# Kernel optimization log

Hardware: AMD Instinct MI355X
Metric: run time of the kernel (lower is better)

The kernel has to match this reference:

```python
import jax, jax.numpy as jnp
import numpy as np

L = 20        # num layers (TTS LM)
Q = 512       # query length
PAST = 512    # past_kv_len
END = PAST + Q  # end_step = 1024
MAXS = 2048   # max_seq_len
D = 896       # hidden size
NKV = 2       # KV heads
NQ = 14       # Q heads
G = NQ // NKV # GQA repeat = 7
HD = 64       # head dim
FF = 4864     # SwiGLU intermediate (Qwen2.5-0.5B)
EPS = 1e-6
SCALE = 1.0 / np.sqrt(HD)


def rms_norm(x, w):
    return x * jax.lax.rsqrt(jnp.mean(x * x, axis=-1, keepdims=True) + EPS) * w


def rotate_half(x):
    x1, x2 = jnp.split(x, 2, axis=-1)
    return jnp.concatenate([-x2, x1], axis=-1)


def setup_inputs() -> dict:
    key = jax.random.key(0)
    ks = jax.random.split(key, 24)
    s = 0.02
    inp = {
        'hidden_states': jax.random.normal(ks[0], (1, Q, D), jnp.float32),
        'position_cos': jax.random.uniform(ks[1], (1, Q, HD), jnp.float32, -1.0, 1.0),
        'position_sin': jax.random.uniform(ks[2], (1, Q, HD), jnp.float32, -1.0, 1.0),
        'attention_mask': jnp.zeros((1, 1, Q, END), jnp.float32),
        'inject_mode': jnp.zeros((1,), jnp.float32),
        'inject_k': jax.random.normal(ks[3], (1, L * NKV, Q, HD), jnp.float32),
        'inject_v': jax.random.normal(ks[4], (1, L * NKV, Q, HD), jnp.float32),
        'k_cache': (jax.random.normal(ks[5], (L, 1, NKV, MAXS, HD), jnp.float32) * 0.5).astype(jnp.float16),
        'v_cache': (jax.random.normal(ks[6], (L, 1, NKV, MAXS, HD), jnp.float32) * 0.5).astype(jnp.float16),
        'Wq': jax.random.normal(ks[7], (L, D, NQ * HD), jnp.float32) * s,
        'bq': jax.random.normal(ks[8], (L, NQ * HD), jnp.float32) * s,
        'Wk': jax.random.normal(ks[9], (L, D, NKV * HD), jnp.float32) * s,
        'bk': jax.random.normal(ks[10], (L, NKV * HD), jnp.float32) * s,
        'Wv': jax.random.normal(ks[11], (L, D, NKV * HD), jnp.float32) * s,
        'bv': jax.random.normal(ks[12], (L, NKV * HD), jnp.float32) * s,
        'Wo': jax.random.normal(ks[13], (L, NQ * HD, D), jnp.float32) * s,
        'ln1': jnp.ones((L, D), jnp.float32),
        'ln2': jnp.ones((L, D), jnp.float32),
        'Wg': jax.random.normal(ks[14], (L, D, FF), jnp.float32) * s,
        'Wu': jax.random.normal(ks[15], (L, D, FF), jnp.float32) * s,
        'Wd': jax.random.normal(ks[16], (L, FF, D), jnp.float32) * s,
        'final_w': jnp.ones((D,), jnp.float32),
    }
    return inp


def reference(hidden_states, position_cos, position_sin, attention_mask,
              inject_mode, inject_k, inject_v, k_cache, v_cache,
              Wq, bq, Wk, bk, Wv, bv, Wo, ln1, ln2, Wg, Wu, Wd, final_w):
    cos = position_cos[:, None]   # [1,1,Q,HD]
    sin = position_sin[:, None]
    inj = inject_mode[0]
    normal = 1.0 - inj
    mask = attention_mask[:, None]  # [1,1,1,Q,END] broadcast over (g,h)
    # per-layer inject slices: [L,1,NKV,Q,HD]
    ik = jnp.transpose(inject_k.reshape(1, L, NKV, Q, HD), (1, 0, 2, 3, 4))
    iv = jnp.transpose(inject_v.reshape(1, L, NKV, Q, HD), (1, 0, 2, 3, 4))

    def layer_fn(h, p):
        (wq, bq_, wk, bk_, wv, bv_, wo, l1, l2, wg, wu, wd, kc, vc, ikl, ivl) = p
        residual = h
        x = rms_norm(h, l1)
        q = (x @ wq + bq_).reshape(1, Q, NQ, HD).transpose(0, 2, 1, 3)   # [1,NQ,Q,HD]
        k = (x @ wk + bk_).reshape(1, Q, NKV, HD).transpose(0, 2, 1, 3)  # [1,NKV,Q,HD]
        v = (x @ wv + bv_).reshape(1, Q, NKV, HD).transpose(0, 2, 1, 3)
        q = q * cos + rotate_half(q) * sin
        k = k * cos + rotate_half(k) * sin
        k = normal * k + inj * ikl
        v = normal * v + inj * ivl
        kc = kc.at[:, :, PAST:END].set(k.astype(jnp.float16))
        vc = vc.at[:, :, PAST:END].set(v.astype(jnp.float16))
        kf = kc[:, :, :END].astype(jnp.float32)  # [1,NKV,END,HD]
        vf = vc[:, :, :END].astype(jnp.float32)
        qg = q.reshape(1, NKV, G, Q, HD)         # grouped GQA (== repeat_kv)
        scores = jnp.einsum('bghqd,bgkd->bghqk', qg, kf) * SCALE + mask
        w = jax.nn.softmax(scores, axis=-1)
        o = jnp.einsum('bghqk,bgkd->bghqd', w, vf)
        o = o.reshape(1, NQ, Q, HD).transpose(0, 2, 1, 3).reshape(1, Q, NQ * HD)
        h = residual + o @ wo
        residual = h
        x = rms_norm(h, l2)
        h = residual + (jax.nn.silu(x @ wg) * (x @ wu)) @ wd
        return h, None

    xs = (Wq, bq, Wk, bk, Wv, bv, Wo, ln1, ln2, Wg, Wu, Wd, k_cache, v_cache, ik, iv)
    h, _ = jax.lax.scan(layer_fn, hidden_states, xs)
    return rms_norm(h, final_w)
```

## Files before the change

kernel.cpp:

```cpp
#include <hip/hip_runtime.h>
#include <hip/hip_fp16.h>
#include <hip/hip_cooperative_groups.h>

namespace cg = cooperative_groups;

#define NLAYER 20
#define QLEN 512
#define PAST 512
#define ENDS 1024
#define MAXS 2048
#define DMODEL 896
#define NKV 2
#define NQ 14
#define GQ 7
#define HD 64
#define FF 4864
#define RMSEPS 1e-6f
#define ATT_SCALE 0.125f

typedef _Float16 f16x8 __attribute__((ext_vector_type(8)));
typedef float f32x4 __attribute__((ext_vector_type(4)));
typedef unsigned int u32_;

__device__ __forceinline__ void gld16(const void* g, void* l) {
    __builtin_amdgcn_global_load_lds(
        (const __attribute__((address_space(1))) u32_*)g,
        (__attribute__((address_space(3))) u32_*)l, 16, 0, 0);
}

union SmemU {
    struct { __half As[8192]; __half Bs[8192]; } g;
    struct { __half S[16512]; float rowinv[16]; } a;
    struct { float T[32][33]; } p;
    struct { float red[4]; } r;
};

__device__ __forceinline__ void gemm_body(
    const __half* __restrict__ A, int lda, const __half* __restrict__ B, int ldb,
    float* __restrict__ outP, __half* __restrict__ actP, int N, int Kps, int mode,
    int bx, int by, int bz, int t, __half* As, __half* Bs)
{
    const int lane = t & 63, wave = t >> 6;
    const int wm = wave >> 1, wn = wave & 1;
    const int m0 = by * 128, n0 = bx * 128;
    const int kb0 = bz * Kps;
    const int sr = t >> 2, sc = (t & 3) * 8;
    const int la = lane & 15, ka = (lane >> 4) * 8;
    const int nIter = Kps >> 5;
    const int swzS = ((sr >> 1) & 3) << 3;
    const int scw = sc ^ swzS;
    const size_t a0 = (size_t)(m0 + sr) * lda + kb0 + scw;
    const size_t a1 = (size_t)(m0 + sr + 64) * lda + kb0 + scw;
    const size_t b0 = (size_t)(n0 + sr) * ldb + kb0 + scw;
    const size_t b1 = (size_t)(n0 + sr + 64) * ldb + kb0 + scw;
    const int l0 = sr * 32 + sc, l1 = (sr + 64) * 32 + sc;

    f32x4 acc[4][4] = {};
    gld16(&A[a0], &As[l0]);
    gld16(&A[a1], &As[l1]);
    gld16(&B[b0], &Bs[l0]);
    gld16(&B[b1], &Bs[l1]);
    int buf = 0;
    for (int kt = 0; kt < nIter; kt++) {
        __syncthreads();
        if (kt + 1 < nIter) {
            const int ko = (kt + 1) * 32;
            gld16(&A[a0 + ko], &As[(buf ^ 1) * 4096 + l0]);
            gld16(&A[a1 + ko], &As[(buf ^ 1) * 4096 + l1]);
            gld16(&B[b0 + ko], &Bs[(buf ^ 1) * 4096 + l0]);
            gld16(&B[b1 + ko], &Bs[(buf ^ 1) * 4096 + l1]);
        }
        f16x8 av[4], bv[4];
#pragma unroll
        for (int i = 0; i < 4; i++) {
            const int row = wm * 64 + i * 16 + la;
            av[i] = *(const f16x8*)&As[buf * 4096 + row * 32 + (ka ^ (((row >> 1) & 3) << 3))];
        }
#pragma unroll
        for (int j = 0; j < 4; j++) {
            const int row = wn * 64 + j * 16 + la;
            bv[j] = *(const f16x8*)&Bs[buf * 4096 + row * 32 + (ka ^ (((row >> 1) & 3) << 3))];
        }
#pragma unroll
        for (int i = 0; i < 4; i++)
#pragma unroll
            for (int j = 0; j < 4; j++)
                acc[i][j] = __builtin_amdgcn_mfma_f32_16x16x32_f16(av[i], bv[j], acc[i][j], 0, 0, 0);
        buf ^= 1;
    }
    __syncthreads();
    const int r0 = m0 + wm * 64 + (lane >> 4) * 4;
    const int c0 = n0 + wn * 64 + la;
    if (mode == 0) {
        float* o = outP + (size_t)bz * QLEN * N;
#pragma unroll
        for (int i = 0; i < 4; i++)
#pragma unroll
            for (int j = 0; j < 4; j++)
#pragma unroll
                for (int r = 0; r < 4; r++)
                    o[(size_t)(r0 + i * 16 + r) * N + c0 + j * 16] = acc[i][j][r];
    } else {
#pragma unroll
        for (int i = 0; i < 4; i++)
#pragma unroll
            for (int j = 0; j < 4; j++)
#pragma unroll
                for (int r = 0; r < 4; r++) {
                    float v = acc[i][j][r];
                    float other = __shfl_xor(v, 1);
                    if (!(la & 1)) {
                        const int c = c0 + j * 16;
                        const int row = r0 + i * 16 + r;
                        float sg = v / (1.f + __expf(-v));
                        actP[(size_t)row * FF + (c >> 1)] = __float2half(sg * other);
                    }
                }
    }
}

__device__ __forceinline__ void prep_body(
    const float* __restrict__ Wq, const float* __restrict__ Wk, const float* __restrict__ Wv,
    const float* __restrict__ Wo, const float* __restrict__ Wg, const float* __restrict__ Wu,
    const float* __restrict__ Wd, int layer, int z, int bx, int t, float (*T)[33],
    __half* __restrict__ dstW)
{
    const int K = (z == 3) ? FF : DMODEL;
    const int N = (z == 0) ? 1152 : (z == 2) ? 2 * FF : DMODEL;
    const int tilesN = N / 32;
    const int tk = bx / tilesN, tn = bx % tilesN;
    const int k0 = tk * 32, n0 = tn * 32;
    const float* src; int ldn, nc0; int isU = 0;
    if (z == 0) {
        if (n0 < 896)       { src = Wq + (size_t)layer * 896 * 896; ldn = 896; nc0 = n0; }
        else if (n0 < 1024) { src = Wk + (size_t)layer * 896 * 128; ldn = 128; nc0 = n0 - 896; }
        else                { src = Wv + (size_t)layer * 896 * 128; ldn = 128; nc0 = n0 - 1024; }
    } else if (z == 1) { src = Wo + (size_t)layer * 896 * 896; ldn = 896; nc0 = n0; }
    else if (z == 2) {
        if (n0 < FF) { src = Wg + (size_t)layer * 896 * FF; ldn = FF; nc0 = n0; }
        else         { src = Wu + (size_t)layer * 896 * FF; ldn = FF; nc0 = n0 - FF; isU = 1; }
    } else { src = Wd + (size_t)layer * FF * 896; ldn = 896; nc0 = n0; }

    __syncthreads();
    const int r = t >> 3, c4 = (t & 7) * 4;
    float4 v = *(const float4*)&src[(size_t)(k0 + r) * ldn + nc0 + c4];
    T[r][c4 + 0] = v.x; T[r][c4 + 1] = v.y; T[r][c4 + 2] = v.z; T[r][c4 + 3] = v.w;
    __syncthreads();
    const int drow = (z == 2) ? (2 * (nc0 + r) + isU) : (n0 + r);
    __half* dst = dstW + (size_t)drow * K + k0 + c4;
    __half2 p0 = __halves2half2(__float2half_rn(T[c4 + 0][r]), __float2half_rn(T[c4 + 1][r]));
    __half2 p1 = __halves2half2(__float2half_rn(T[c4 + 2][r]), __float2half_rn(T[c4 + 3][r]));
    *(__half2*)dst = p0;
    *(__half2*)(dst + 2) = p1;
    __syncthreads();
}

__device__ __forceinline__ void prep_dispatch(
    const float* Wq, const float* Wk, const float* Wv, const float* Wo,
    const float* Wg, const float* Wu, const float* Wd,
    const float* bq, const float* bk, const float* bv,
    int layer, int j, int t, float (*T)[33],
    __half* wq, __half* wo, __half* wgu, __half* wd, float* bqkv)
{
    int z; __half* dst; int bx = j;
    if (j < 1008)       { z = 0; dst = wq; }
    else if (j < 1792)  { z = 1; dst = wo;  bx -= 1008; }
    else if (j < 10304) { z = 2; dst = wgu; bx -= 1792; }
    else                { z = 3; dst = wd;  bx -= 10304; }
    prep_body(Wq, Wk, Wv, Wo, Wg, Wu, Wd, layer, z, bx, t, T, dst);
    if (z == 0 && bx == 0) {
        for (int i = t; i < 1152; i += 256) {
            float b = (i < 896) ? bq[(size_t)layer * 896 + i]
                    : (i < 1024) ? bk[(size_t)layer * 128 + i - 896]
                                 : bv[(size_t)layer * 128 + i - 1024];
            bqkv[i] = b;
        }
    }
}

__device__ __forceinline__ void ropekv_body(
    const float* __restrict__ part, const float* __restrict__ bias,
    const float* __restrict__ cosb, const float* __restrict__ sinb,
    const float* __restrict__ injm, const float* __restrict__ injk,
    const float* __restrict__ injv, const float* __restrict__ kc32,
    const float* __restrict__ vc32, int layer, int nsplit,
    __half* __restrict__ qr, __half* __restrict__ Ka, __half* __restrict__ Vt,
    int p, int lt)
{
    const int kvh = lt >> 6, d = lt & 63;
    if (p < PAST) {
        const size_t idx = (((size_t)layer * NKV + kvh) * MAXS + p) * HD + d;
        Ka[((size_t)kvh * ENDS + p) * HD + d] = __float2half(kc32[idx]);
        Vt[((size_t)kvh * HD + d) * ENDS + p] = __float2half(vc32[idx]);
        return;
    }
    const int pn = p - PAST;
    const float inj = injm[0], nrm = 1.f - inj;
    const float* rb = part + (size_t)pn * 1152;
    const size_t sst = (size_t)QLEN * 1152;
    auto rsum = [&](int c) {
        float x = bias[c];
        for (int s = 0; s < nsplit; s++) x += rb[(size_t)s * sst + c];
        return x;
    };
    for (int idx = lt; idx < NQ * HD; idx += 128) {
        const int dd = idx & 63;
        float x = rsum(idx);
        int pc = (dd < 32) ? idx + 32 : idx - 32;
        float pv = rsum(pc);
        if (dd < 32) pv = -pv;
        float rv = x * cosb[pn * HD + dd] + pv * sinb[pn * HD + dd];
        qr[((size_t)(idx >> 6) * QLEN + pn) * HD + dd] = __float2half(rv);
    }
    {
        const int c = NQ * HD + lt;
        float x = rsum(c);
        int pc = (d < 32) ? c + 32 : c - 32;
        float pv = rsum(pc);
        if (d < 32) pv = -pv;
        float rv = x * cosb[pn * HD + d] + pv * sinb[pn * HD + d];
        float kn = nrm * rv + inj * injk[(((size_t)layer * NKV + kvh) * QLEN + pn) * HD + d];
        Ka[((size_t)kvh * ENDS + PAST + pn) * HD + d] = __float2half(kn);
        const int cv = NQ * HD + NKV * HD + lt;
        float vv = rsum(cv);
        float vn = nrm * vv + inj * injv[(((size_t)layer * NKV + kvh) * QLEN + pn) * HD + d];
        Vt[((size_t)kvh * HD + d) * ENDS + PAST + pn] = __float2half(vn);
    }
}

__device__ __forceinline__ int sswz(int row, int col) {
    return row * 1032 + (col ^ ((row & 7) << 3));
}

__device__ __forceinline__ void attn_body(
    const __half* __restrict__ qr, const __half* __restrict__ Ka,
    const __half* __restrict__ Vt, const float* __restrict__ mask,
    __half* __restrict__ ob, int q0, int h, int t, __half* S, float* rowinv)
{
    const int kv = h / GQ;
    const int lane = t & 63, w = t >> 6;
    const int la = lane & 15, kg = lane >> 4;

    const f16x8* qp = (const f16x8*)&qr[((size_t)h * QLEN + q0 + la) * HD + kg * 8];
    const f16x8 qa0 = qp[0], qa1 = qp[4];
    __syncthreads();

    for (int kb = 0; kb < 256; kb += 16) {
        const int key = w * 256 + kb + la;
        const f16x8* kp = (const f16x8*)&Ka[((size_t)kv * ENDS + key) * HD + kg * 8];
        f32x4 s4 = {0.f, 0.f, 0.f, 0.f};
        s4 = __builtin_amdgcn_mfma_f32_16x16x32_f16(qa0, kp[0], s4, 0, 0, 0);
        s4 = __builtin_amdgcn_mfma_f32_16x16x32_f16(qa1, kp[4], s4, 0, 0, 0);
#pragma unroll
        for (int r = 0; r < 4; r++) {
            const int row = kg * 4 + r;
            float sv = s4[r] * ATT_SCALE + mask[(size_t)(q0 + row) * ENDS + key];
            S[sswz(row, key)] = __float2half(sv);
        }
    }
    __syncthreads();
    {
        const int row = w * 4 + kg;
        float mx = -1e30f;
        for (int j = 0; j < 64; j++)
            mx = fmaxf(mx, __half2float(S[sswz(row, la + 16 * j)]));
        for (int o = 1; o < 16; o <<= 1) mx = fmaxf(mx, __shfl_xor(mx, o));
        float sum = 0.f;
        for (int j = 0; j < 64; j++) {
            const int idx = sswz(row, la + 16 * j);
            float e = __expf(__half2float(S[idx]) - mx);
            S[idx] = __float2half(e);
            sum += e;
        }
        for (int o = 1; o < 16; o <<= 1) sum += __shfl_xor(sum, o);
        if (la == 0) rowinv[row] = 1.f / sum;
    }
    __syncthreads();
    {
        const int d = 16 * w + la;
        const __half* vrow = &Vt[((size_t)kv * HD + d) * ENDS];
        f32x4 acc = {0.f, 0.f, 0.f, 0.f};
        for (int ks = 0; ks < ENDS; ks += 32) {
            f16x8 pa = *(const f16x8*)&S[sswz(la, ks + kg * 8)];
            f16x8 vb = *(const f16x8*)&vrow[ks + kg * 8];
            acc = __builtin_amdgcn_mfma_f32_16x16x32_f16(pa, vb, acc, 0, 0, 0);
        }
#pragma unroll
        for (int r = 0; r < 4; r++) {
            const int qrow = kg * 4 + r;
            ob[(size_t)(q0 + qrow) * (NQ * HD) + h * HD + d] =
                __float2half(acc[r] * rowinv[qrow]);
        }
    }
    __syncthreads();
}

__device__ inline void cvt_store(float* p, float v)  { *p = v; }
__device__ inline void cvt_store(__half* p, float v) { *p = __float2half(v); }

template <typename OUT>
__device__ __forceinline__ void rms_body(
    float* __restrict__ h, const float* __restrict__ parts, int nparts,
    const float* __restrict__ w, OUT* __restrict__ out, int m, int t,
    float* red, float scale)
{
    float loc[4];
    float ss = 0.f;
    int r = 0;
    for (int i = t; i < DMODEL; i += 256, r++) {
        float x = h[(size_t)m * DMODEL + i];
        for (int s = 0; s < nparts; s++)
            x += parts[(size_t)s * QLEN * DMODEL + (size_t)m * DMODEL + i];
        loc[r] = x;
        if (nparts) h[(size_t)m * DMODEL + i] = x;
        ss += x * x;
    }
    for (int o = 32; o; o >>= 1) ss += __shfl_xor(ss, o);
    if ((t & 63) == 0) red[t >> 6] = ss;
    __syncthreads();
    float rs = rsqrtf((red[0] + red[1] + red[2] + red[3]) / (float)DMODEL + RMSEPS);
    r = 0;
    for (int i = t; i < DMODEL; i += 256, r++)
        cvt_store(&out[(size_t)m * DMODEL + i], loc[r] * rs * w[i] * scale);
    __syncthreads();
}

struct P22 {
    const float *hidden, *cosb, *sinb, *mask, *injm, *injk, *injv, *kc32, *vc32;
    const float *Wq, *bq, *Wk, *bk, *Wv, *bv, *Wo, *ln1, *ln2, *Wg, *Wu, *Wd, *finw;
    float *h; __half *xn, *qr, *Ka, *Vt, *ob, *act; float *BIGR;
    float *bqkv0, *bqkv1;
    __half *wq0, *wo0, *wgu0, *wd0, *wq1, *wo1, *wgu1, *wd1;
    float *outF;
};

#define PC_RMS1 512
#define PC_QKV  880
#define PC_ROPE 512
#define PC_ATTN 2304
#define PC_O    1824
#define PC_RMS2 1024
#define PC_GU   5904
#define PC_D    1600
#define PB_RMS1 0
#define PB_QKV  512
#define PB_ROPE 1392
#define PB_ATTN 1904
#define PB_O    4208
#define PB_RMS2 6032
#define PB_GU   7056
#define PB_D    12960

__global__ __launch_bounds__(256) void mega_kernel(P22 P)
{
    __shared__ SmemU sm;
    cg::grid_group gg = cg::this_grid();
    const int nb = gridDim.x, bid = blockIdx.x, t = threadIdx.x;

    for (int j = bid; j < 1792; j += nb) {
        int i = j * 256 + t;
        if (i < QLEN * DMODEL) P.h[i] = P.hidden[i];
    }
    for (int j = bid; j < 14560; j += nb)
        prep_dispatch(P.Wq, P.Wk, P.Wv, P.Wo, P.Wg, P.Wu, P.Wd, P.bq, P.bk, P.bv,
                      0, j, t, sm.p.T, P.wq0, P.wo0, P.wgu0, P.wd0, P.bqkv0);
    gg.sync();

    for (int l = 0; l < NLAYER; l++) {
        const int pb = l & 1;
        const __half* wq  = pb ? P.wq1  : P.wq0;
        const __half* wo  = pb ? P.wo1  : P.wo0;
        const __half* wgu = pb ? P.wgu1 : P.wgu0;
        const __half* wd  = pb ? P.wd1  : P.wd0;
        const float*  bqk = pb ? P.bqkv1 : P.bqkv0;
        const bool hasN = (l + 1 < NLAYER);
        __half* nwq  = pb ? P.wq0  : P.wq1;
        __half* nwo  = pb ? P.wo0  : P.wo1;
        __half* nwgu = pb ? P.wgu0 : P.wgu1;
        __half* nwd  = pb ? P.wd0  : P.wd1;
        float*  nbq  = pb ? P.bqkv0 : P.bqkv1;
        #define PREPN(idx) prep_dispatch(P.Wq, P.Wk, P.Wv, P.Wo, P.Wg, P.Wu, P.Wd, \
            P.bq, P.bk, P.bv, l + 1, (idx), t, sm.p.T, nwq, nwo, nwgu, nwd, nbq)

        for (int j = bid; j < QLEN + (hasN ? PC_RMS1 : 0); j += nb) {
            if (j < QLEN)
                rms_body<__half>(P.h, l ? P.BIGR : nullptr, l ? 8 : 0,
                                 P.ln1 + (size_t)l * DMODEL, P.xn, j, t, sm.r.red, 1.f);
            else PREPN(PB_RMS1 + j - QLEN);
        }
        gg.sync();

        for (int j = bid; j < 144 + (hasN ? PC_QKV : 0); j += nb) {
            if (j < 144) {
                int z = j / 36, r = j % 36;
                gemm_body(P.xn, DMODEL, wq, DMODEL, P.BIGR, nullptr, 1152, 224, 0,
                          r % 9, r / 9, z, t, sm.g.As, sm.g.Bs);
            } else PREPN(PB_QKV + j - 144);
        }
        gg.sync();

        for (int j = bid; j < 512 + (hasN ? PC_ROPE : 0); j += nb) {
            if (j < 512)
                ropekv_body(P.BIGR, bqk, P.cosb, P.sinb, P.injm, P.injk, P.injv,
                            P.kc32, P.vc32, l, 4, P.qr, P.Ka, P.Vt,
                            j * 2 + (t >> 7), t & 127);
            else PREPN(PB_ROPE + j - 512);
        }
        gg.sync();

        for (int j = bid; j < 448 + (hasN ? PC_ATTN : 0); j += nb) {
            if (j < 448)
                attn_body(P.qr, P.Ka, P.Vt, P.mask, P.ob, (j & 31) * 16, j >> 5, t,
                          sm.a.S, sm.a.rowinv);
            else PREPN(PB_ATTN + j - 448);
        }
        gg.sync();

        for (int j = bid; j < 112 + (hasN ? PC_O : 0); j += nb) {
            if (j < 112) {
                int z = j / 28, r = j % 28;
                gemm_body(P.ob, DMODEL, wo, DMODEL, P.BIGR, nullptr, DMODEL, 224, 0,
                          r % 7, r / 7, z, t, sm.g.As, sm.g.Bs);
            } else PREPN(PB_O + j - 112);
        }
        gg.sync();

        for (int j = bid; j < QLEN + (hasN ? PC_RMS2 : 0); j += nb) {
            if (j < QLEN)
                rms_body<__half>(P.h, P.BIGR, 4, P.ln2 + (size_t)l * DMODEL, P.xn,
                                 j, t, sm.r.red, 1.f);
            else PREPN(PB_RMS2 + j - QLEN);
        }
        gg.sync();

        for (int j = bid; j < 304 + (hasN ? PC_GU : 0); j += nb) {
            if (j < 304)
                gemm_body(P.xn, DMODEL, wgu, DMODEL, nullptr, P.act, 2 * FF, DMODEL, 1,
                          j % 76, j / 76, 0, t, sm.g.As, sm.g.Bs);
            else PREPN(PB_GU + j - 304);
        }
        gg.sync();

        for (int j = bid; j < 224 + (hasN ? PC_D : 0); j += nb) {
            if (j < 224) {
                int z = j / 28, r = j % 28;
                gemm_body(P.act, FF, wd, FF, P.BIGR, nullptr, DMODEL, 608, 0,
                          r % 7, r / 7, z, t, sm.g.As, sm.g.Bs);
            } else PREPN(PB_D + j - 224);
        }
        gg.sync();
        #undef PREPN
    }
    for (int j = bid; j < QLEN; j += nb)
        rms_body<float>(P.h, P.BIGR, 8, P.finw, P.outF, j, t, sm.r.red, 1.f);
}

__global__ __launch_bounds__(256) void init_kernel(
    const float* __restrict__ hidden, float* __restrict__ h, int* __restrict__ flags)
{
    const int idx = blockIdx.x * 256 + threadIdx.x;
    if (blockIdx.x == 0 && threadIdx.x < 8) flags[threadIdx.x] = 0;
    if (idx < QLEN * DMODEL) h[idx] = hidden[idx];
}

__global__ __launch_bounds__(256) void prep_all(
    const float* Wq, const float* Wk, const float* Wv, const float* Wo,
    const float* Wg, const float* Wu, const float* Wd,
    const float* bq, const float* bk, const float* bv, int layer,
    __half* wqkv, __half* wo, __half* wgu, __half* wd, float* bqkv)
{
    __shared__ float T[32][33];
    prep_dispatch(Wq, Wk, Wv, Wo, Wg, Wu, Wd, bq, bk, bv, layer, blockIdx.x,
                  threadIdx.x, T, wqkv, wo, wgu, wd, bqkv);
}

__global__ __launch_bounds__(256) void gemm128(
    const __half* A, int lda, const __half* B, int ldb,
    float* outP, __half* actP, int N, int Kps, int mode)
{
    __shared__ SmemU sm;
    gemm_body(A, lda, B, ldb, outP, actP, N, Kps, mode,
              blockIdx.x, blockIdx.y, blockIdx.z, threadIdx.x, sm.g.As, sm.g.Bs);
}

__global__ __launch_bounds__(128) void ropekv_kernel(
    const float* part, const float* bias, const float* cosb, const float* sinb,
    const float* injm, const float* injk, const float* injv,
    const float* kc32, const float* vc32, int layer, int nsplit,
    __half* qr, __half* Ka, __half* Vt)
{
    ropekv_body(part, bias, cosb, sinb, injm, injk, injv, kc32, vc32,
                layer, nsplit, qr, Ka, Vt, blockIdx.x, threadIdx.x);
}

__global__ __launch_bounds__(256) void attn_mfma(
    const __half* qr, const __half* Ka, const __half* Vt, const float* mask, __half* ob)
{
    __shared__ SmemU sm;
    attn_body(qr, Ka, Vt, mask, ob, blockIdx.x * 16, blockIdx.y, threadIdx.x,
              sm.a.S, sm.a.rowinv);
}

template <typename OUT>
__global__ __launch_bounds__(256) void rms_kernel(
    float* h, const float* parts, int nparts, const float* w, OUT* out,
    const int* flags)
{
    __shared__ float red[4];
    float scale = 1.f;
    if (flags) {
        int E = flags[1];
        for (int i = 0; i < E; i++) scale *= 3.f;
    }
    rms_body<OUT>(h, parts, nparts, w, out, blockIdx.x, threadIdx.x, red, scale);
}

__global__ __launch_bounds__(256) void check_gemm(
    const __half* A, int lda, const __half* B, int K,
    const float* part, int N, int nz, int* flags)
{
    const int t = threadIdx.x;
    const int m = (t >> 4) * 33;
    const int n = ((t & 15) * 997) % N;
    float acc = 0.f;
    for (int k = 0; k < K; k++)
        acc += __half2float(A[(size_t)m * lda + k]) * __half2float(B[(size_t)n * K + k]);
    float got = 0.f;
    for (int z = 0; z < nz; z++) got += part[(size_t)z * QLEN * N + (size_t)m * N + n];
    if (fabsf(acc - got) > 0.03f) atomicOr(&flags[1], 1);
}

extern "C" void kernel_launch(void* const* d_in, const int* in_sizes, int n_in,
                              void* d_out, int out_size, void* d_ws, size_t ws_size,
                              hipStream_t stream)
{
    const float*  hidden = (const float*)d_in[0];
    const float*  cosb   = (const float*)d_in[1];
    const float*  sinb   = (const float*)d_in[2];
    const float*  mask   = (const float*)d_in[3];
    const float*  injm   = (const float*)d_in[4];
    const float*  injk   = (const float*)d_in[5];
    const float*  injv   = (const float*)d_in[6];
    const float*  kc32   = (const float*)d_in[7];
    const float*  vc32   = (const float*)d_in[8];
    const float*  Wq     = (const float*)d_in[9];
    const float*  bq     = (const float*)d_in[10];
    const float*  Wk     = (const float*)d_in[11];
    const float*  bk     = (const float*)d_in[12];
    const float*  Wv     = (const float*)d_in[13];
    const float*  bv     = (const float*)d_in[14];
    const float*  Wo     = (const float*)d_in[15];
    const float*  ln1    = (const float*)d_in[16];
    const float*  ln2    = (const float*)d_in[17];
    const float*  Wg     = (const float*)d_in[18];
    const float*  Wu     = (const float*)d_in[19];
    const float*  Wd     = (const float*)d_in[20];
    const float*  finw   = (const float*)d_in[21];

    bool size_ok = (n_in == 22) &&
        in_sizes[0] == 458752 && in_sizes[1] == 32768 && in_sizes[3] == 524288 &&
        in_sizes[4] == 1 && in_sizes[5] == 1310720 && in_sizes[7] == 5242880 &&
        in_sizes[9] == 16056320 && in_sizes[10] == 17920 && in_sizes[11] == 2293760 &&
        in_sizes[15] == 16056320 && in_sizes[16] == 17920 && in_sizes[18] == 87162880 &&
        in_sizes[20] == 87162880 && in_sizes[21] == 896;
    if (!size_ok) { hipMemsetAsync(d_out, 0x42, (size_t)out_size * 4, stream); return; }

    char* ws = (char*)d_ws;
    size_t off = 0;
    auto alloc = [&](size_t bytes) { void* p = ws + off; off += (bytes + 255) & ~255ull; return p; };
    int*    flags = (int*)alloc(256);
    float*  bqkv0 = (float*)alloc(1152 * 4);
    float*  bqkv1 = (float*)alloc(1152 * 4);
    float*  h     = (float*)alloc((size_t)QLEN * DMODEL * 4);
    __half* xn    = (__half*)alloc((size_t)QLEN * DMODEL * 2);
    __half* qr    = (__half*)alloc((size_t)NQ * QLEN * HD * 2);
    __half* Ka    = (__half*)alloc((size_t)NKV * ENDS * HD * 2);
    __half* Vt    = (__half*)alloc((size_t)NKV * ENDS * HD * 2);
    __half* ob    = (__half*)alloc((size_t)QLEN * NQ * HD * 2);
    __half* act   = (__half*)alloc((size_t)QLEN * FF * 2);
    float*  BIGR  = (float*)alloc(8ull * QLEN * 1152 * 4);
    __half* wq0   = (__half*)alloc(2064384);
    __half* wo0   = (__half*)alloc(1605632);
    __half* wgu0  = (__half*)alloc(17432576);
    __half* wd0   = (__half*)alloc(8716288);
    const size_t NEED_LEGACY = off;
    __half* wq1   = (__half*)alloc(2064384);
    __half* wo1   = (__half*)alloc(1605632);
    __half* wgu1  = (__half*)alloc(17432576);
    __half* wd1   = (__half*)alloc(8716288);
    const size_t NEED_MEGA = off;

    if (ws_size < NEED_LEGACY) {
        hipMemsetAsync(d_out, 0, (size_t)out_size * 4, stream);
        return;
    }

    bool mega_ok = (ws_size >= NEED_MEGA);
    if (mega_ok) {
        int maxB = 0;
        hipError_t e = hipOccupancyMaxActiveBlocksPerMultiprocessor(
            &maxB, reinterpret_cast<const void*>(&mega_kernel), 256, 0);
        if (e != hipSuccess || maxB < 1) mega_ok = false;
        if (mega_ok) {
            int grid = maxB * 256;
            if (grid > 1024) grid = 1024;
            P22 Pv = { hidden, cosb, sinb, mask, injm, injk, injv, kc32, vc32,
                       Wq, bq, Wk, bk, Wv, bv, Wo, ln1, ln2, Wg, Wu, Wd, finw,
                       h, xn, qr, Ka, Vt, ob, act, BIGR, bqkv0, bqkv1,
                       wq0, wo0, wgu0, wd0, wq1, wo1, wgu1, wd1, (float*)d_out };
            void* args[] = { (void*)&Pv };
            hipError_t le = hipLaunchCooperativeKernel(
                reinterpret_cast<const void*>(&mega_kernel),
                dim3(grid), dim3(256), args, 0, stream);
            if (le == hipSuccess) return;
            mega_ok = false;
        }
    }

    init_kernel<<<1792, 256, 0, stream>>>(hidden, h, flags);
    for (int l = 0; l < NLAYER; l++) {
        prep_all<<<14560, 256, 0, stream>>>(Wq, Wk, Wv, Wo, Wg, Wu, Wd, bq, bk, bv, l,
                                            wq0, wo0, wgu0, wd0, bqkv0);
        rms_kernel<__half><<<QLEN, 256, 0, stream>>>(h, l ? BIGR : nullptr, l ? 8 : 0,
                                                     ln1 + (size_t)l * DMODEL, xn, nullptr);
        gemm128<<<dim3(9, 4, 4), 256, 0, stream>>>(xn, DMODEL, wq0, DMODEL, BIGR, nullptr, 1152, 224, 0);
        if (l == 0) check_gemm<<<1, 256, 0, stream>>>(xn, DMODEL, wq0, DMODEL, BIGR, 1152, 4, flags);
        ropekv_kernel<<<ENDS, 128, 0, stream>>>(BIGR, bqkv0, cosb, sinb, injm, injk, injv,
                                                kc32, vc32, l, 4, qr, Ka, Vt);
        attn_mfma<<<dim3(32, 14), 256, 0, stream>>>(qr, Ka, Vt, mask, ob);
        gemm128<<<dim3(7, 4, 4), 256, 0, stream>>>(ob, DMODEL, wo0, DMODEL, BIGR, nullptr, DMODEL, 224, 0);
        rms_kernel<__half><<<QLEN, 256, 0, stream>>>(h, BIGR, 4, ln2 + (size_t)l * DMODEL, xn, nullptr);
        gemm128<<<dim3(76, 4, 1), 256, 0, stream>>>(xn, DMODEL, wgu0, DMODEL, nullptr, act, 2 * FF, DMODEL, 1);
        gemm128<<<dim3(7, 4, 8), 256, 0, stream>>>(act, FF, wd0, FF, BIGR, nullptr, DMODEL, 608, 0);
    }
    rms_kernel<float><<<QLEN, 256, 0, stream>>>(h, BIGR, 8, finw, (float*)d_out, flags);
}
```

Measured before the change: 3.005 ms.

## Fuse RoPE/KV epilogue into QKV GEMM and enlarge weight-prep tiles

```diff
diff --git a/kernel.cpp b/kernel.cpp
--- a/kernel.cpp
+++ b/kernel.cpp
@@ -31,64 +31,65 @@
 union SmemU {
     struct { __half As[8192]; __half Bs[8192]; } g;
     struct { __half S[16512]; float rowinv[16]; } a;
-    struct { float T[32][33]; } p;
+    struct { float T[32][129]; } p;
     struct { float red[4]; } r;
 };
+
+#define GEMM_STAGE_SETUP(A_, lda_, B_, ldb_, Kps_)                              \
+    const int lane = t & 63, wave = t >> 6;                                     \
+    const int wm = wave >> 1, wn = wave & 1;                                    \
+    const int m0 = by * 128, n0 = bx * 128;                                     \
+    const int kb0 = bz * (Kps_);                                                \
+    const int sr = t >> 2, sc = (t & 3) * 8;                                    \
+    const int la = lane & 15, ka = (lane >> 4) * 8;                             \
+    const int nIter = (Kps_) >> 5;                                              \
+    const int scw = sc ^ (((sr >> 1) & 3) << 3);                                \
+    const size_t a0 = (size_t)(m0 + sr) * (lda_) + kb0 + scw;                   \
+    const size_t a1 = (size_t)(m0 + sr + 64) * (lda_) + kb0 + scw;              \
+    const size_t b0 = (size_t)(n0 + sr) * (ldb_) + kb0 + scw;                   \
+    const size_t b1 = (size_t)(n0 + sr + 64) * (ldb_) + kb0 + scw;              \
+    const int l0 = sr * 32 + sc, l1 = (sr + 64) * 32 + sc;                      \
+    f32x4 acc[4][4] = {};                                                       \
+    gld16(&(A_)[a0], &As[l0]);                                                  \
+    gld16(&(A_)[a1], &As[l1]);                                                  \
+    gld16(&(B_)[b0], &Bs[l0]);                                                  \
+    gld16(&(B_)[b1], &Bs[l1]);                                                  \
+    int buf = 0;                                                                \
+    for (int kt = 0; kt < nIter; kt++) {                                        \
+        __syncthreads();                                                        \
+        if (kt + 1 < nIter) {                                                   \
+            const int ko = (kt + 1) * 32;                                       \
+            gld16(&(A_)[a0 + ko], &As[(buf ^ 1) * 4096 + l0]);                  \
+            gld16(&(A_)[a1 + ko], &As[(buf ^ 1) * 4096 + l1]);                  \
+            gld16(&(B_)[b0 + ko], &Bs[(buf ^ 1) * 4096 + l0]);                  \
+            gld16(&(B_)[b1 + ko], &Bs[(buf ^ 1) * 4096 + l1]);                  \
+        }                                                                       \
+        f16x8 av[4], bv[4];                                                     \
+        _Pragma("unroll")                                                       \
+        for (int i = 0; i < 4; i++) {                                           \
+            const int row = wm * 64 + i * 16 + la;                              \
+            av[i] = *(const f16x8*)&As[buf * 4096 + row * 32 + (ka ^ (((row >> 1) & 3) << 3))]; \
+        }                                                                       \
+        _Pragma("unroll")                                                       \
+        for (int j = 0; j < 4; j++) {                                           \
+            const int row = wn * 64 + j * 16 + la;                              \
+            bv[j] = *(const f16x8*)&Bs[buf * 4096 + row * 32 + (ka ^ (((row >> 1) & 3) << 3))]; \
+        }                                                                       \
+        _Pragma("unroll")                                                       \
+        for (int i = 0; i < 4; i++)                                             \
+            _Pragma("unroll")                                                   \
+            for (int j = 0; j < 4; j++)                                         \
+                acc[i][j] = __builtin_amdgcn_mfma_f32_16x16x32_f16(av[i], bv[j], acc[i][j], 0, 0, 0); \
+        buf ^= 1;                                                               \
+    }                                                                           \
+    __syncthreads();
 
 __device__ __forceinline__ void gemm_body(
     const __half* __restrict__ A, int lda, const __half* __restrict__ B, int ldb,
     float* __restrict__ outP, __half* __restrict__ actP, int N, int Kps, int mode,
     int bx, int by, int bz, int t, __half* As, __half* Bs)
 {
-    const int lane = t & 63, wave = t >> 6;
-    const int wm = wave >> 1, wn = wave & 1;
-    const int m0 = by * 128, n0 = bx * 128;
-    const int kb0 = bz * Kps;
-    const int sr = t >> 2, sc = (t & 3) * 8;
-    const int la = lane & 15, ka = (lane >> 4) * 8;
-    const int nIter = Kps >> 5;
-    const int swzS = ((sr >> 1) & 3) << 3;
-    const int scw = sc ^ swzS;
-    const size_t a0 = (size_t)(m0 + sr) * lda + kb0 + scw;
-    const size_t a1 = (size_t)(m0 + sr + 64) * lda + kb0 + scw;
-    const size_t b0 = (size_t)(n0 + sr) * ldb + kb0 + scw;
-    const size_t b1 = (size_t)(n0 + sr + 64) * ldb + kb0 + scw;
-    const int l0 = sr * 32 + sc, l1 = (sr + 64) * 32 + sc;
-
-    f32x4 acc[4][4] = {};
-    gld16(&A[a0], &As[l0]);
-    gld16(&A[a1], &As[l1]);
-    gld16(&B[b0], &Bs[l0]);
-    gld16(&B[b1], &Bs[l1]);
-    int buf = 0;
-    for (int kt = 0; kt < nIter; kt++) {
-        __syncthreads();
-        if (kt + 1 < nIter) {
-            const int ko = (kt + 1) * 32;
-            gld16(&A[a0 + ko], &As[(buf ^ 1) * 4096 + l0]);
-            gld16(&A[a1 + ko], &As[(buf ^ 1) * 4096 + l1]);
-            gld16(&B[b0 + ko], &Bs[(buf ^ 1) * 4096 + l0]);
-            gld16(&B[b1 + ko], &Bs[(buf ^ 1) * 4096 + l1]);
-        }
-        f16x8 av[4], bv[4];
-#pragma unroll
-        for (int i = 0; i < 4; i++) {
-            const int row = wm * 64 + i * 16 + la;
-            av[i] = *(const f16x8*)&As[buf * 4096 + row * 32 + (ka ^ (((row >> 1) & 3) << 3))];
-        }
-#pragma unroll
-        for (int j = 0; j < 4; j++) {
-            const int row = wn * 64 + j * 16 + la;
-            bv[j] = *(const f16x8*)&Bs[buf * 4096 + row * 32 + (ka ^ (((row >> 1) & 3) << 3))];
-        }
-#pragma unroll
-        for (int i = 0; i < 4; i++)
-#pragma unroll
-            for (int j = 0; j < 4; j++)
-                acc[i][j] = __builtin_amdgcn_mfma_f32_16x16x32_f16(av[i], bv[j], acc[i][j], 0, 0, 0);
-        buf ^= 1;
-    }
-    __syncthreads();
+    GEMM_STAGE_SETUP(A, lda, B, ldb, Kps)
     const int r0 = m0 + wm * 64 + (lane >> 4) * 4;
     const int c0 = n0 + wn * 64 + la;
     if (mode == 0) {
@@ -119,22 +120,64 @@
     }
 }
 
+__device__ __forceinline__ void gemm_qkv_body(
+    const __half* __restrict__ A, const __half* __restrict__ B,
+    const float* __restrict__ bqkv, const float* __restrict__ cosb,
+    const float* __restrict__ sinb, float inj,
+    const float* __restrict__ injk, const float* __restrict__ injv,
+    __half* __restrict__ qr, __half* __restrict__ Ka, __half* __restrict__ Vt,
+    int layer, int bx, int by, int t, __half* As, __half* Bs)
+{
+    const int bz = 0;
+    GEMM_STAGE_SETUP(A, DMODEL, B, DMODEL, 896)
+    const int r0 = m0 + wm * 64 + (lane >> 4) * 4;
+    const int c0 = n0 + wn * 64 + la;
+    const float nrm = 1.f - inj;
+#pragma unroll
+    for (int i = 0; i < 4; i++)
+#pragma unroll
+        for (int j = 0; j < 4; j++)
+#pragma unroll
+            for (int r = 0; r < 4; r++) {
+                const int pn = r0 + i * 16 + r;
+                const int c = c0 + j * 16;
+                const int d = c & 63;
+                float v = acc[i][j][r] + bqkv[c];
+                if (c < 1024) {
+                    float pvv = acc[i][j ^ 2][r] + bqkv[c ^ 32];
+                    float rot = (d < 32) ? -pvv : pvv;
+                    float rv = v * cosb[pn * HD + d] + rot * sinb[pn * HD + d];
+                    if (c < 896) {
+                        qr[((size_t)(c >> 6) * QLEN + pn) * HD + d] = __float2half(rv);
+                    } else {
+                        const int kvh = (c - 896) >> 6;
+                        float kn = nrm * rv + inj * injk[(((size_t)layer * NKV + kvh) * QLEN + pn) * HD + d];
+                        Ka[((size_t)kvh * ENDS + PAST + pn) * HD + d] = __float2half(kn);
+                    }
+                } else {
+                    const int kvh = (c - 1024) >> 6;
+                    float vn = nrm * v + inj * injv[(((size_t)layer * NKV + kvh) * QLEN + pn) * HD + d];
+                    Vt[((size_t)kvh * HD + d) * ENDS + PAST + pn] = __float2half(vn);
+                }
+            }
+}
+
 __device__ __forceinline__ void prep_body(
     const float* __restrict__ Wq, const float* __restrict__ Wk, const float* __restrict__ Wv,
     const float* __restrict__ Wo, const float* __restrict__ Wg, const float* __restrict__ Wu,
-    const float* __restrict__ Wd, int layer, int z, int bx, int t, float (*T)[33],
+    const float* __restrict__ Wd, int layer, int z, int bx, int t, float (*T)[129],
     __half* __restrict__ dstW)
 {
     const int K = (z == 3) ? FF : DMODEL;
     const int N = (z == 0) ? 1152 : (z == 2) ? 2 * FF : DMODEL;
-    const int tilesN = N / 32;
+    const int tilesN = N / 128;
     const int tk = bx / tilesN, tn = bx % tilesN;
-    const int k0 = tk * 32, n0 = tn * 32;
+    const int k0 = tk * 32, n0 = tn * 128;
     const float* src; int ldn, nc0; int isU = 0;
     if (z == 0) {
-        if (n0 < 896)       { src = Wq + (size_t)layer * 896 * 896; ldn = 896; nc0 = n0; }
-        else if (n0 < 1024) { src = Wk + (size_t)layer * 896 * 128; ldn = 128; nc0 = n0 - 896; }
-        else                { src = Wv + (size_t)layer * 896 * 128; ldn = 128; nc0 = n0 - 1024; }
+        if (n0 < 896)        { src = Wq + (size_t)layer * 896 * 896; ldn = 896; nc0 = n0; }
+        else if (n0 < 1024)  { src = Wk + (size_t)layer * 896 * 128; ldn = 128; nc0 = n0 - 896; }
+        else                 { src = Wv + (size_t)layer * 896 * 128; ldn = 128; nc0 = n0 - 1024; }
     } else if (z == 1) { src = Wo + (size_t)layer * 896 * 896; ldn = 896; nc0 = n0; }
     else if (z == 2) {
         if (n0 < FF) { src = Wg + (size_t)layer * 896 * FF; ldn = FF; nc0 = n0; }
@@ -142,16 +185,28 @@
     } else { src = Wd + (size_t)layer * FF * 896; ldn = 896; nc0 = n0; }
 
     __syncthreads();
-    const int r = t >> 3, c4 = (t & 7) * 4;
-    float4 v = *(const float4*)&src[(size_t)(k0 + r) * ldn + nc0 + c4];
-    T[r][c4 + 0] = v.x; T[r][c4 + 1] = v.y; T[r][c4 + 2] = v.z; T[r][c4 + 3] = v.w;
-    __syncthreads();
-    const int drow = (z == 2) ? (2 * (nc0 + r) + isU) : (n0 + r);
-    __half* dst = dstW + (size_t)drow * K + k0 + c4;
-    __half2 p0 = __halves2half2(__float2half_rn(T[c4 + 0][r]), __float2half_rn(T[c4 + 1][r]));
-    __half2 p1 = __halves2half2(__float2half_rn(T[c4 + 2][r]), __float2half_rn(T[c4 + 3][r]));
-    *(__half2*)dst = p0;
-    *(__half2*)(dst + 2) = p1;
+    {
+        const int r = t >> 3, cb = (t & 7) * 16;
+        const float* s = &src[(size_t)(k0 + r) * ldn + nc0 + cb];
+#pragma unroll
+        for (int q = 0; q < 4; q++) {
+            float4 v = *(const float4*)&s[q * 4];
+            T[r][cb + q * 4 + 0] = v.x; T[r][cb + q * 4 + 1] = v.y;
+            T[r][cb + q * 4 + 2] = v.z; T[r][cb + q * 4 + 3] = v.w;
+        }
+    }
+    __syncthreads();
+    {
+        const int nr = t >> 1, kh = (t & 1) * 16;
+        const int drow = (z == 2) ? (2 * (nc0 + nr) + isU) : (n0 + nr);
+        __half tmp[16];
+#pragma unroll
+        for (int kk = 0; kk < 16; kk++)
+            tmp[kk] = __float2half_rn(T[kh + kk][nr]);
+        __half* dst = dstW + (size_t)drow * K + k0 + kh;
+        *(uint4*)dst = *(const uint4*)&tmp[0];
+        *(uint4*)(dst + 8) = *(const uint4*)&tmp[8];
+    }
     __syncthreads();
 }
 
@@ -159,14 +214,14 @@
     const float* Wq, const float* Wk, const float* Wv, const float* Wo,
     const float* Wg, const float* Wu, const float* Wd,
     const float* bq, const float* bk, const float* bv,
-    int layer, int j, int t, float (*T)[33],
+    int layer, int j, int t, float (*T)[129],
     __half* wq, __half* wo, __half* wgu, __half* wd, float* bqkv)
 {
     int z; __half* dst; int bx = j;
-    if (j < 1008)       { z = 0; dst = wq; }
-    else if (j < 1792)  { z = 1; dst = wo;  bx -= 1008; }
-    else if (j < 10304) { z = 2; dst = wgu; bx -= 1792; }
-    else                { z = 3; dst = wd;  bx -= 10304; }
+    if (j < 252)        { z = 0; dst = wq; }
+    else if (j < 448)   { z = 1; dst = wo;  bx -= 252; }
+    else if (j < 2576)  { z = 2; dst = wgu; bx -= 448; }
+    else                { z = 3; dst = wd;  bx -= 2576; }
     prep_body(Wq, Wk, Wv, Wo, Wg, Wu, Wd, layer, z, bx, t, T, dst);
     if (z == 0 && bx == 0) {
         for (int i = t; i < 1152; i += 256) {
@@ -176,6 +231,16 @@
             bqkv[i] = b;
         }
     }
+}
+
+__device__ __forceinline__ void cache_copy_body(
+    const float* __restrict__ kc32, const float* __restrict__ vc32, int layer,
+    __half* __restrict__ Ka, __half* __restrict__ Vt, int p, int lt)
+{
+    const int kvh = lt >> 6, d = lt & 63;
+    const size_t idx = (((size_t)layer * NKV + kvh) * MAXS + p) * HD + d;
+    Ka[((size_t)kvh * ENDS + p) * HD + d] = __float2half(kc32[idx]);
+    Vt[((size_t)kvh * HD + d) * ENDS + p] = __float2half(vc32[idx]);
 }
 
 __device__ __forceinline__ void ropekv_body(
@@ -188,12 +253,7 @@
     int p, int lt)
 {
     const int kvh = lt >> 6, d = lt & 63;
-    if (p < PAST) {
-        const size_t idx = (((size_t)layer * NKV + kvh) * MAXS + p) * HD + d;
-        Ka[((size_t)kvh * ENDS + p) * HD + d] = __float2half(kc32[idx]);
-        Vt[((size_t)kvh * HD + d) * ENDS + p] = __float2half(vc32[idx]);
-        return;
-    }
+    if (p < PAST) { cache_copy_body(kc32, vc32, layer, Ka, Vt, p, lt); return; }
     const int pn = p - PAST;
     const float inj = injm[0], nrm = 1.f - inj;
     const float* rb = part + (size_t)pn * 1152;
@@ -334,34 +394,33 @@
     float *outF;
 };
 
-#define PC_RMS1 512
-#define PC_QKV  880
-#define PC_ROPE 512
-#define PC_ATTN 2304
-#define PC_O    1824
-#define PC_RMS2 1024
-#define PC_GU   5904
-#define PC_D    1600
-#define PB_RMS1 0
-#define PB_QKV  512
-#define PB_ROPE 1392
-#define PB_ATTN 1904
-#define PB_O    4208
-#define PB_RMS2 6032
-#define PB_GU   7056
-#define PB_D    12960
+#define PC_A 300
+#define PC_B 700
+#define PC_C 576
+#define PC_D 800
+#define PC_E 500
+#define PC_F 600
+#define PC_G 164
+#define PB_A 0
+#define PB_B 300
+#define PB_C 1000
+#define PB_D 1576
+#define PB_E 2376
+#define PB_F 2876
+#define PB_G 3476
 
 __global__ __launch_bounds__(256) void mega_kernel(P22 P)
 {
     __shared__ SmemU sm;
     cg::grid_group gg = cg::this_grid();
     const int nb = gridDim.x, bid = blockIdx.x, t = threadIdx.x;
+    const float inj = P.injm[0];
 
     for (int j = bid; j < 1792; j += nb) {
         int i = j * 256 + t;
         if (i < QLEN * DMODEL) P.h[i] = P.hidden[i];
     }
-    for (int j = bid; j < 14560; j += nb)
+    for (int j = bid; j < 3640; j += nb)
         prep_dispatch(P.Wq, P.Wk, P.Wv, P.Wo, P.Wg, P.Wu, P.Wd, P.bq, P.bk, P.bv,
                       0, j, t, sm.p.T, P.wq0, P.wo0, P.wgu0, P.wd0, P.bqkv0);
     gg.sync();
@@ -382,71 +441,64 @@
         #define PREPN(idx) prep_dispatch(P.Wq, P.Wk, P.Wv, P.Wo, P.Wg, P.Wu, P.Wd, \
             P.bq, P.bk, P.bv, l + 1, (idx), t, sm.p.T, nwq, nwo, nwgu, nwd, nbq)
 
-        for (int j = bid; j < QLEN + (hasN ? PC_RMS1 : 0); j += nb) {
+        for (int j = bid; j < QLEN + (hasN ? PC_A : 0); j += nb) {
             if (j < QLEN)
                 rms_body<__half>(P.h, l ? P.BIGR : nullptr, l ? 8 : 0,
                                  P.ln1 + (size_t)l * DMODEL, P.xn, j, t, sm.r.red, 1.f);
-            else PREPN(PB_RMS1 + j - QLEN);
+            else PREPN(PB_A + j - QLEN);
         }
         gg.sync();
 
-        for (int j = bid; j < 144 + (hasN ? PC_QKV : 0); j += nb) {
-            if (j < 144) {
-                int z = j / 36, r = j % 36;
-                gemm_body(P.xn, DMODEL, wq, DMODEL, P.BIGR, nullptr, 1152, 224, 0,
-                          r % 9, r / 9, z, t, sm.g.As, sm.g.Bs);
-            } else PREPN(PB_QKV + j - 144);
+        for (int j = bid; j < 292 + (hasN ? PC_B : 0); j += nb) {
+            if (j < 36)
+                gemm_qkv_body(P.xn, wq, bqk, P.cosb, P.sinb, inj, P.injk, P.injv,
+                              P.qr, P.Ka, P.Vt, l, j % 9, j / 9, t, sm.g.As, sm.g.Bs);
+            else if (j < 292) {
+                int p = (j - 36) * 2 + (t >> 7);
+                cache_copy_body(P.kc32, P.vc32, l, P.Ka, P.Vt, p, t & 127);
+            } else PREPN(PB_B + j - 292);
         }
         gg.sync();
 
-        for (int j = bid; j < 512 + (hasN ? PC_ROPE : 0); j += nb) {
-            if (j < 512)
-                ropekv_body(P.BIGR, bqk, P.cosb, P.sinb, P.injm, P.injk, P.injv,
-                            P.kc32, P.vc32, l, 4, P.qr, P.Ka, P.Vt,
-                            j * 2 + (t >> 7), t & 127);
-            else PREPN(PB_ROPE + j - 512);
-        }
-        gg.sync();
-
-        for (int j = bid; j < 448 + (hasN ? PC_ATTN : 0); j += nb) {
+        for (int j = bid; j < 448 + (hasN ? PC_C : 0); j += nb) {
             if (j < 448)
                 attn_body(P.qr, P.Ka, P.Vt, P.mask, P.ob, (j & 31) * 16, j >> 5, t,
                           sm.a.S, sm.a.rowinv);
-            else PREPN(PB_ATTN + j - 448);
+            else PREPN(PB_C + j - 448);
         }
         gg.sync();
 
-        for (int j = bid; j < 112 + (hasN ? PC_O : 0); j += nb) {
+        for (int j = bid; j < 112 + (hasN ? PC_D : 0); j += nb) {
             if (j < 112) {
                 int z = j / 28, r = j % 28;
                 gemm_body(P.ob, DMODEL, wo, DMODEL, P.BIGR, nullptr, DMODEL, 224, 0,
                           r % 7, r / 7, z, t, sm.g.As, sm.g.Bs);
-            } else PREPN(PB_O + j - 112);
+            } else PREPN(PB_D + j - 112);
         }
         gg.sync();
 
-        for (int j = bid; j < QLEN + (hasN ? PC_RMS2 : 0); j += nb) {
+        for (int j = bid; j < QLEN + (hasN ? PC_E : 0); j += nb) {
             if (j < QLEN)
                 rms_body<__half>(P.h, P.BIGR, 4, P.ln2 + (size_t)l * DMODEL, P.xn,
                                  j, t, sm.r.red, 1.f);
-            else PREPN(PB_RMS2 + j - QLEN);
+            else PREPN(PB_E + j - QLEN);
         }
         gg.sync();
 
-        for (int j = bid; j < 304 + (hasN ? PC_GU : 0); j += nb) {
+        for (int j = bid; j < 304 + (hasN ? PC_F : 0); j += nb) {
             if (j < 304)
                 gemm_body(P.xn, DMODEL, wgu, DMODEL, nullptr, P.act, 2 * FF, DMODEL, 1,
                           j % 76, j / 76, 0, t, sm.g.As, sm.g.Bs);
-            else PREPN(PB_GU + j - 304);
+            else PREPN(PB_F + j - 304);
         }
         gg.sync();
 
-        for (int j = bid; j < 224 + (hasN ? PC_D : 0); j += nb) {
+        for (int j = bid; j < 224 + (hasN ? PC_G : 0); j += nb) {
             if (j < 224) {
                 int z = j / 28, r = j % 28;
                 gemm_body(P.act, FF, wd, FF, P.BIGR, nullptr, DMODEL, 608, 0,
                           r % 7, r / 7, z, t, sm.g.As, sm.g.Bs);
-            } else PREPN(PB_D + j - 224);
+            } else PREPN(PB_G + j - 224);
         }
         gg.sync();
         #undef PREPN
@@ -469,7 +521,7 @@
     const float* bq, const float* bk, const float* bv, int layer,
     __half* wqkv, __half* wo, __half* wgu, __half* wd, float* bqkv)
 {
-    __shared__ float T[32][33];
+    __shared__ float T[32][129];
     prep_dispatch(Wq, Wk, Wv, Wo, Wg, Wu, Wd, bq, bk, bv, layer, blockIdx.x,
                   threadIdx.x, T, wqkv, wo, wgu, wd, bqkv);
 }
@@ -507,27 +559,7 @@
     const int* flags)
 {
     __shared__ float red[4];
-    float scale = 1.f;
-    if (flags) {
-        int E = flags[1];
-        for (int i = 0; i < E; i++) scale *= 3.f;
-    }
-    rms_body<OUT>(h, parts, nparts, w, out, blockIdx.x, threadIdx.x, red, scale);
-}
-
-__global__ __launch_bounds__(256) void check_gemm(
-    const __half* A, int lda, const __half* B, int K,
-    const float* part, int N, int nz, int* flags)
-{
-    const int t = threadIdx.x;
-    const int m = (t >> 4) * 33;
-    const int n = ((t & 15) * 997) % N;
-    float acc = 0.f;
-    for (int k = 0; k < K; k++)
-        acc += __half2float(A[(size_t)m * lda + k]) * __half2float(B[(size_t)n * K + k]);
-    float got = 0.f;
-    for (int z = 0; z < nz; z++) got += part[(size_t)z * QLEN * N + (size_t)m * N + n];
-    if (fabsf(acc - got) > 0.03f) atomicOr(&flags[1], 1);
+    rms_body<OUT>(h, parts, nparts, w, out, blockIdx.x, threadIdx.x, red, 1.f);
 }
 
 extern "C" void kernel_launch(void* const* d_in, const int* in_sizes, int n_in,
@@ -619,12 +651,11 @@
 
     init_kernel<<<1792, 256, 0, stream>>>(hidden, h, flags);
     for (int l = 0; l < NLAYER; l++) {
-        prep_all<<<14560, 256, 0, stream>>>(Wq, Wk, Wv, Wo, Wg, Wu, Wd, bq, bk, bv, l,
-                                            wq0, wo0, wgu0, wd0, bqkv0);
+        prep_all<<<3640, 256, 0, stream>>>(Wq, Wk, Wv, Wo, Wg, Wu, Wd, bq, bk, bv, l,
+                                           wq0, wo0, wgu0, wd0, bqkv0);
         rms_kernel<__half><<<QLEN, 256, 0, stream>>>(h, l ? BIGR : nullptr, l ? 8 : 0,
                                                      ln1 + (size_t)l * DMODEL, xn, nullptr);
         gemm128<<<dim3(9, 4, 4), 256, 0, stream>>>(xn, DMODEL, wq0, DMODEL, BIGR, nullptr, 1152, 224, 0);
-        if (l == 0) check_gemm<<<1, 256, 0, stream>>>(xn, DMODEL, wq0, DMODEL, BIGR, 1152, 4, flags);
         ropekv_kernel<<<ENDS, 128, 0, stream>>>(BIGR, bqkv0, cosb, sinb, injm, injk, injv,
                                                 kc32, vc32, l, 4, qr, Ka, Vt);
         attn_mfma<<<dim3(32, 14), 256, 0, stream>>>(qr, Ka, Vt, mask, ob);
@@ -633,5 +664,5 @@
         gemm128<<<dim3(76, 4, 1), 256, 0, stream>>>(xn, DMODEL, wgu0, DMODEL, nullptr, act, 2 * FF, DMODEL, 1);
         gemm128<<<dim3(7, 4, 8), 256, 0, stream>>>(act, FF, wd0, FF, BIGR, nullptr, DMODEL, 608, 0);
     }
-    rms_kernel<float><<<QLEN, 256, 0, stream>>>(h, BIGR, 8, finw, (float*)d_out, flags);
-}
+    rms_kernel<float><<<QLEN, 256, 0, stream>>>(h, BIGR, 8, finw, (float*)d_out, nullptr);
+}
```

Measured after the change: 2.887 ms. 1.04x faster.
